# Performance work log

Hardware: AMD Instinct MI355X
Metric: run time of the kernel (lower is better)

## Reference

```python
import jax, jax.numpy as jnp
import numpy as np

N_NODES = 100000
N_EDGES = 1600000
IN_C, HID_C, OUT_C, N_CLS = 128, 128, 128, 40


def setup_inputs() -> dict:
    key = jax.random.key(0)
    ks = jax.random.split(key, 10)
    x = jax.random.normal(ks[0], (N_NODES, IN_C), dtype=jnp.float32)
    edge_index = jax.random.randint(ks[1], (2, N_EDGES), 0, N_NODES, dtype=jnp.int64)
    s = 1.0 / np.sqrt(IN_C)
    W_self1 = jax.random.uniform(ks[2], (IN_C, HID_C), jnp.float32, -s, s)
    W_neigh1 = jax.random.uniform(ks[3], (IN_C, HID_C), jnp.float32, -s, s)
    b1 = jnp.zeros((HID_C,), jnp.float32)
    s2 = 1.0 / np.sqrt(HID_C)
    W_self2 = jax.random.uniform(ks[4], (HID_C, OUT_C), jnp.float32, -s2, s2)
    W_neigh2 = jax.random.uniform(ks[5], (HID_C, OUT_C), jnp.float32, -s2, s2)
    b2 = jnp.zeros((OUT_C,), jnp.float32)
    s3 = 1.0 / np.sqrt(OUT_C)
    W_cls = jax.random.uniform(ks[6], (OUT_C, N_CLS), jnp.float32, -s3, s3)
    b_cls = jax.random.uniform(ks[7], (N_CLS,), jnp.float32, -s3, s3)
    return dict(x=x, edge_index=edge_index, W_self1=W_self1, W_neigh1=W_neigh1, b1=b1,
                W_self2=W_self2, W_neigh2=W_neigh2, b2=b2, W_cls=W_cls, b_cls=b_cls)


def _mean_agg(h, src, dst, n_nodes):
    # sum of in-neighbor features per destination node, then divide by in-degree
    sums = jax.ops.segment_sum(h[src], dst, num_segments=n_nodes)  # [N, F]
    deg = jax.ops.segment_sum(jnp.ones(src.shape[0], h.dtype), dst, num_segments=n_nodes)
    return sums / jnp.maximum(deg, 1.0)[:, None]


def _sage_conv(h, src, dst, W_self, W_neigh, b):
    # DGL mean SAGEConv: fc_self(h) + fc_neigh(mean_neigh(h)) + bias
    h_neigh = _mean_agg(h, src, dst, h.shape[0])
    return h @ W_self + h_neigh @ W_neigh + b


def reference(x, edge_index, W_self1, W_neigh1, b1, W_self2, W_neigh2, b2, W_cls, b_cls):
    src, dst = edge_index[0], edge_index[1]
    h = jax.nn.relu(_sage_conv(x, src, dst, W_self1, W_neigh1, b1))
    h = jax.nn.relu(_sage_conv(h, src, dst, W_self2, W_neigh2, b2))
    return h @ W_cls + b_cls
```

## Files before the change

### kernel.cpp

```cpp
#include <hip/hip_runtime.h>

#define N_NODES 100000
#define N_EDGES 1600000
#define C 128
#define NCLS 40
#define NBUCK 196
#define BCAP 12288
#define NT_TILES 3125

typedef _Float16 half8 __attribute__((ext_vector_type(8)));
typedef float f32x4 __attribute__((ext_vector_type(4)));
typedef float f32x16 __attribute__((ext_vector_type(16)));


__global__ __launch_bounds__(256) void bucket_scatter_k(const int* __restrict__ src,
    const int* __restrict__ dst, int* __restrict__ bucket_cnt, int* __restrict__ bucketArr) {
  __shared__ int lh[NBUCK], lbase[NBUCK], lcur[NBUCK];
  int tid = threadIdx.x;
  for (int i = tid; i < NBUCK; i += 256) { lh[i] = 0; lcur[i] = 0; }
  __syncthreads();
  int base = blockIdx.x * 4096;
  int bmax = min(base + 4096, N_EDGES);
  for (int e = base + tid; e < bmax; e += 256)
    atomicAdd(&lh[dst[e] >> 9], 1);
  __syncthreads();
  for (int i = tid; i < NBUCK; i += 256)
    lbase[i] = lh[i] ? atomicAdd(&bucket_cnt[i], lh[i]) : 0;
  __syncthreads();
  for (int e = base + tid; e < bmax; e += 256) {
    int d = dst[e];
    int b = d >> 9, loc = d & 511;
    int p = lbase[b] + atomicAdd(&lcur[b], 1);
    if (p < BCAP) bucketArr[(size_t)b * BCAP + p] = (src[e] << 9) | loc;
  }
}

__global__ void bucket_scan_k(const int* __restrict__ bucket_cnt, int* __restrict__ bucket_base,
                              int* __restrict__ rp) {
  if (threadIdx.x == 0 && blockIdx.x == 0) {
    int run = 0;
    for (int b = 0; b < NBUCK; b++) {
      bucket_base[b] = run;
      run += min(bucket_cnt[b], BCAP);
    }
    bucket_base[NBUCK] = run;
    rp[N_NODES] = run;
  }
}

__global__ __launch_bounds__(256) void bucket_sort_k(const int* __restrict__ bucketArr,
    const int* __restrict__ bucket_cnt, const int* __restrict__ bucket_base,
    int* __restrict__ rp, int* __restrict__ csr) {
  __shared__ int hist[512], offs[512], curs[512];
  __shared__ int wpart[4];
  __shared__ int lsrc[BCAP];
  int b = blockIdx.x, tid = threadIdx.x;
  int cnt = min(bucket_cnt[b], BCAP);
  int base = bucket_base[b];
  for (int i = tid; i < 512; i += 256) hist[i] = 0;
  __syncthreads();
  for (int i = tid; i < cnt; i += 256)
    atomicAdd(&hist[bucketArr[(size_t)b * BCAP + i] & 511], 1);
  __syncthreads();
  int a0 = hist[2 * tid], a1 = hist[2 * tid + 1];
  int s = a0 + a1;
  int lane = tid & 63, wid = tid >> 6;
  int inc = s;
  for (int d = 1; d < 64; d <<= 1) { int y = __shfl_up(inc, d, 64); if (lane >= d) inc += y; }
  if (lane == 63) wpart[wid] = inc;
  __syncthreads();
  int woff = 0;
  for (int q = 0; q < wid; q++) woff += wpart[q];
  int ex = woff + inc - s;
  offs[2 * tid] = ex; offs[2 * tid + 1] = ex + a0;
  curs[2 * tid] = ex; curs[2 * tid + 1] = ex + a0;
  __syncthreads();
  for (int i = tid; i < 512; i += 256) {
    int gn = b * 512 + i;
    if (gn < N_NODES) rp[gn] = base + offs[i];
  }
  for (int i = tid; i < cnt; i += 256) {
    int packed = bucketArr[(size_t)b * BCAP + i];
    int p = atomicAdd(&curs[packed & 511], 1);
    lsrc[p] = packed >> 9;
  }
  __syncthreads();
  for (int i = tid; i < cnt; i += 256) csr[base + i] = lsrc[i];
}


__global__ __launch_bounds__(256) void f32_to_f16_k(const float* __restrict__ in,
                                                    _Float16* __restrict__ out) {
  int i = blockIdx.x * 256 + threadIdx.x;
  float4 v0 = *(const float4*)(in + (size_t)i * 8);
  float4 v1 = *(const float4*)(in + (size_t)i * 8 + 4);
  half8 o;
  o[0] = (_Float16)v0.x; o[1] = (_Float16)v0.y; o[2] = (_Float16)v0.z; o[3] = (_Float16)v0.w;
  o[4] = (_Float16)v1.x; o[5] = (_Float16)v1.y; o[6] = (_Float16)v1.z; o[7] = (_Float16)v1.w;
  *(half8*)(out + (size_t)i * 8) = o;
}

__global__ void build_wt_k(const float* __restrict__ Ws, const float* __restrict__ Wn,
                           _Float16* __restrict__ WT) {
  int n = blockIdx.x, k = threadIdx.x;
  float v = (k < 128) ? Ws[k * 128 + n] : Wn[(k - 128) * 128 + n];
  WT[n * 256 + k] = (_Float16)v;
}

__global__ void build_wct_k(const float* __restrict__ Wc, const float* __restrict__ bc,
                            _Float16* __restrict__ WcT, float* __restrict__ bcf) {
  int c = blockIdx.x, k = threadIdx.x;
  float v = (c < NCLS) ? Wc[k * NCLS + c] : 0.f;
  WcT[c * C + k] = (_Float16)v;
  if (k == 0) bcf[c] = (c < NCLS) ? bc[c] : 0.f;
}


__global__ __launch_bounds__(256) void agg_mean_h_k(const _Float16* __restrict__ feat,
    const int* __restrict__ rp, const int* __restrict__ csr, _Float16* __restrict__ out) {
  int w = threadIdx.x >> 6;
  int node = blockIdx.x * 4 + w;
  int lane = threadIdx.x & 63;
  int g = lane >> 4, lr = lane & 15;
  int beg = rp[node], end = rp[node + 1];
  float acc[8] = {}, acc2[8] = {};
  int j = beg;
  for (; j + 8 <= end; j += 8) {
    int e0 = csr[j + g];
    int e1 = csr[j + 4 + g];
    half8 v0 = *(const half8*)(feat + (size_t)e0 * C + lr * 8);
    half8 v1 = *(const half8*)(feat + (size_t)e1 * C + lr * 8);
#pragma unroll
    for (int q = 0; q < 8; q++) { acc[q] += (float)v0[q]; acc2[q] += (float)v1[q]; }
  }
  for (; j + 4 <= end; j += 4) {
    int e0 = csr[j + g];
    half8 v0 = *(const half8*)(feat + (size_t)e0 * C + lr * 8);
#pragma unroll
    for (int q = 0; q < 8; q++) acc[q] += (float)v0[q];
  }
  int rem = end - j;
  if (g < rem) {
    int e0 = csr[j + g];
    half8 v0 = *(const half8*)(feat + (size_t)e0 * C + lr * 8);
#pragma unroll
    for (int q = 0; q < 8; q++) acc2[q] += (float)v0[q];
  }
#pragma unroll
  for (int q = 0; q < 8; q++) {
    float v = acc[q] + acc2[q];
    v += __shfl_xor(v, 16, 64);
    v += __shfl_xor(v, 32, 64);
    acc[q] = v;
  }
  if (g == 0) {
    float inv = 1.0f / fmaxf((float)(end - beg), 1.0f);
    half8 o;
#pragma unroll
    for (int q = 0; q < 8; q++) o[q] = (_Float16)(acc[q] * inv);
    *(half8*)(out + (size_t)node * C + lr * 8) = o;
  }
}


__global__ __launch_bounds__(256) void sage_gemm_ws_k(
    const _Float16* __restrict__ Xs, const _Float16* __restrict__ Xn,
    const _Float16* __restrict__ WT, const float* __restrict__ bias,
    _Float16* __restrict__ out) {
  __shared__ _Float16 cbuf[32][136];
  int tid = threadIdx.x, lane = tid & 63, wid = tid >> 6;
  int l31 = lane & 31, l5 = lane >> 5;
  int col0 = wid * 32;

  half8 b[16];
#pragma unroll
  for (int ks = 0; ks < 16; ks++)
    b[ks] = *(const half8*)(WT + (size_t)(col0 + l31) * 256 + ks * 16 + l5 * 8);
  float bcol = bias[col0 + l31];

  for (int t = blockIdx.x; t < NT_TILES; t += gridDim.x) {
    size_t row0 = (size_t)t * 32;
    half8 a[16];
#pragma unroll
    for (int ks = 0; ks < 8; ks++) {
      a[ks]     = *(const half8*)(Xs + (row0 + l31) * C + ks * 16 + l5 * 8);
      a[ks + 8] = *(const half8*)(Xn + (row0 + l31) * C + ks * 16 + l5 * 8);
    }
    f32x16 acc = {};
#pragma unroll
    for (int ks = 0; ks < 16; ks++)
      acc = __builtin_amdgcn_mfma_f32_32x32x16_f16(a[ks], b[ks], acc, 0, 0, 0);

    __syncthreads();
#pragma unroll
    for (int q = 0; q < 16; q++) {
      int row = (q & 3) + 8 * (q >> 2) + 4 * l5;
      float v = fmaxf(acc[q] + bcol, 0.f);
      cbuf[row][col0 + l31] = (_Float16)v;
    }
    __syncthreads();
#pragma unroll
    for (int p = 0; p < 2; p++) {
      int chunk = tid + p * 256;
      int r = chunk >> 4, cg = chunk & 15;
      half8 v = *(const half8*)&cbuf[r][cg * 8];
      *(half8*)(out + (row0 + r) * C + cg * 8) = v;
    }
  }
}


__global__ __launch_bounds__(256) void classifier_mfma_k(const _Float16* __restrict__ h,
    const _Float16* __restrict__ WcT, const float* __restrict__ bcf, float* __restrict__ out) {
  __shared__ float cbuf[64][49];
  int tid = threadIdx.x, lane = tid & 63, wid = tid >> 6;
  int lr = lane & 15, lk = lane >> 4;
  int row0 = blockIdx.x * 64 + wid * 16;
  f32x4 acc[3] = {};
#pragma unroll
  for (int ks = 0; ks < 4; ks++) {
    half8 a = {};
    int r = row0 + lr;
    if (r < N_NODES) a = *(const half8*)(h + (size_t)r * C + ks * 32 + lk * 8);
#pragma unroll
    for (int nf = 0; nf < 3; nf++) {
      half8 bfr = *(const half8*)(WcT + (size_t)(nf * 16 + lr) * C + ks * 32 + lk * 8);
      acc[nf] = __builtin_amdgcn_mfma_f32_16x16x32_f16(a, bfr, acc[nf], 0, 0, 0);
    }
  }
#pragma unroll
  for (int nf = 0; nf < 3; nf++)
#pragma unroll
    for (int q = 0; q < 4; q++) {
      int c = nf * 16 + lr;
      cbuf[wid * 16 + lk * 4 + q][c] = acc[nf][q] + bcf[c];
    }
  __syncthreads();
  int row_blk0 = blockIdx.x * 64;
  for (int i = tid; i < 64 * NCLS; i += 256) {
    int r = i / NCLS, c = i - r * NCLS;
    int gr = row_blk0 + r;
    if (gr < N_NODES) out[(size_t)gr * NCLS + c] = cbuf[r][c];
  }
}


extern "C" void kernel_launch(void* const* d_in, const int* in_sizes, int n_in,
                              void* d_out, int out_size, void* d_ws, size_t ws_size,
                              hipStream_t stream) {
  (void)in_sizes; (void)n_in; (void)out_size; (void)ws_size;
  const float* x   = (const float*)d_in[0];
  const int*   ei  = (const int*)d_in[1];
  const float* Ws1 = (const float*)d_in[2];
  const float* Wn1 = (const float*)d_in[3];
  const float* b1  = (const float*)d_in[4];
  const float* Ws2 = (const float*)d_in[5];
  const float* Wn2 = (const float*)d_in[6];
  const float* b2  = (const float*)d_in[7];
  const float* Wc  = (const float*)d_in[8];
  const float* bc  = (const float*)d_in[9];
  const int* src = ei;
  const int* dst = ei + N_EDGES;

  char* ws = (char*)d_ws;
  size_t off = 0;
  auto alloc = [&](size_t bytes) {
    void* p = ws + off;
    off = (off + bytes + 255) & ~(size_t)255;
    return p;
  };
  int*      bucket_cnt  = (int*)alloc((size_t)NBUCK * 4);
  int*      bucket_base = (int*)alloc((size_t)(NBUCK + 1) * 4);
  int*      bucketArr   = (int*)alloc((size_t)NBUCK * BCAP * 4);
  int*      rp          = (int*)alloc((size_t)(N_NODES + 1) * 4);
  int*      csr         = (int*)alloc((size_t)N_EDGES * 4);
  _Float16* hA          = (_Float16*)alloc((size_t)N_NODES * C * 2);
  _Float16* hB          = (_Float16*)alloc((size_t)N_NODES * C * 2);
  _Float16* hC          = (_Float16*)alloc((size_t)N_NODES * C * 2);
  _Float16* WT1         = (_Float16*)alloc((size_t)C * 256 * 2);
  _Float16* WT2         = (_Float16*)alloc((size_t)C * 256 * 2);
  _Float16* WcT         = (_Float16*)alloc((size_t)48 * C * 2);
  float*    bcf         = (float*)alloc(48 * 4);
  float* outf = (float*)d_out;

  hipMemsetAsync(bucket_cnt, 0, (size_t)NBUCK * 4, stream);
  bucket_scatter_k<<<(N_EDGES + 4095) / 4096, 256, 0, stream>>>(src, dst, bucket_cnt, bucketArr);
  bucket_scan_k<<<1, 64, 0, stream>>>(bucket_cnt, bucket_base, rp);
  bucket_sort_k<<<NBUCK, 256, 0, stream>>>(bucketArr, bucket_cnt, bucket_base, rp, csr);

  build_wt_k<<<C, 256, 0, stream>>>(Ws1, Wn1, WT1);
  build_wt_k<<<C, 256, 0, stream>>>(Ws2, Wn2, WT2);
  build_wct_k<<<48, C, 0, stream>>>(Wc, bc, WcT, bcf);
  f32_to_f16_k<<<(N_NODES * C / 8) / 256, 256, 0, stream>>>(x, hA);

  agg_mean_h_k<<<N_NODES / 4, 256, 0, stream>>>(hA, rp, csr, hB);
  sage_gemm_ws_k<<<782, 256, 0, stream>>>(hA, hB, WT1, b1, hC);
  agg_mean_h_k<<<N_NODES / 4, 256, 0, stream>>>(hC, rp, csr, hB);
  sage_gemm_ws_k<<<782, 256, 0, stream>>>(hC, hB, WT2, b2, hA);
  classifier_mfma_k<<<(N_NODES + 63) / 64, 256, 0, stream>>>(hA, WcT, bcf, outf);
}
```

Measured before the change: 371.8 us.

## Shard mean aggregation by feature column across XCD-mapped blocks; parallelize bucket scan

Result: slower. 436.7 us (+17.4%).

```diff
diff --git a/kernel.cpp b/kernel.cpp
--- a/kernel.cpp
+++ b/kernel.cpp
@@ -21,14 +21,17 @@
   __syncthreads();
   int base = blockIdx.x * 4096;
   int bmax = min(base + 4096, N_EDGES);
-  for (int e = base + tid; e < bmax; e += 256)
-    atomicAdd(&lh[dst[e] >> 9], 1);
+  int dreg[16];
+  int nk = 0;
+  for (int e = base + tid; e < bmax; e += 256) dreg[nk++] = dst[e];
+  for (int k = 0; k < nk; k++) atomicAdd(&lh[dreg[k] >> 9], 1);
   __syncthreads();
   for (int i = tid; i < NBUCK; i += 256)
     lbase[i] = lh[i] ? atomicAdd(&bucket_cnt[i], lh[i]) : 0;
   __syncthreads();
+  nk = 0;
   for (int e = base + tid; e < bmax; e += 256) {
-    int d = dst[e];
+    int d = dreg[nk++];
     int b = d >> 9, loc = d & 511;
     int p = lbase[b] + atomicAdd(&lcur[b], 1);
     if (p < BCAP) bucketArr[(size_t)b * BCAP + p] = (src[e] << 9) | loc;
@@ -37,15 +40,19 @@
 
 __global__ void bucket_scan_k(const int* __restrict__ bucket_cnt, int* __restrict__ bucket_base,
                               int* __restrict__ rp) {
-  if (threadIdx.x == 0 && blockIdx.x == 0) {
-    int run = 0;
-    for (int b = 0; b < NBUCK; b++) {
-      bucket_base[b] = run;
-      run += min(bucket_cnt[b], BCAP);
-    }
-    bucket_base[NBUCK] = run;
-    rp[N_NODES] = run;
-  }
+  int tid = threadIdx.x;
+  int v = (tid < NBUCK) ? min(bucket_cnt[tid], BCAP) : 0;
+  int lane = tid & 63, wid = tid >> 6;
+  int inc = v;
+  for (int d = 1; d < 64; d <<= 1) { int y = __shfl_up(inc, d, 64); if (lane >= d) inc += y; }
+  __shared__ int wsum[4];
+  if (lane == 63) wsum[wid] = inc;
+  __syncthreads();
+  int woff = 0;
+  for (int q = 0; q < wid; q++) woff += wsum[q];
+  int ex = woff + inc - v;
+  if (tid < NBUCK) bucket_base[tid] = ex;
+  if (tid == NBUCK - 1) { bucket_base[NBUCK] = ex + v; rp[N_NODES] = ex + v; }
 }
 
 __global__ __launch_bounds__(256) void bucket_sort_k(const int* __restrict__ bucketArr,
@@ -116,41 +123,48 @@
 }
 
 
-__global__ __launch_bounds__(256) void agg_mean_h_k(const _Float16* __restrict__ feat,
+__global__ __launch_bounds__(256) void agg_mean_shard_k(const _Float16* __restrict__ feat,
     const int* __restrict__ rp, const int* __restrict__ csr, _Float16* __restrict__ out) {
-  int w = threadIdx.x >> 6;
-  int node = blockIdx.x * 4 + w;
-  int lane = threadIdx.x & 63;
-  int g = lane >> 4, lr = lane & 15;
+  int bid = blockIdx.x;
+  int shard = (bid & 7) >> 1;
+  int tile  = (bid >> 3) * 2 + (bid & 1);
+  int tid = threadIdx.x;
+  int w = tid >> 6, lane = tid & 63;
+  int nslot = lane >> 4;
+  int g  = (lane >> 2) & 3;
+  int lr = lane & 3;
+  int node = tile * 16 + w * 4 + nslot;
   int beg = rp[node], end = rp[node + 1];
+  const _Float16* fbase = feat + shard * 32 + lr * 8;
   float acc[8] = {}, acc2[8] = {};
   int j = beg;
   for (; j + 8 <= end; j += 8) {
     int e0 = csr[j + g];
     int e1 = csr[j + 4 + g];
-    half8 v0 = *(const half8*)(feat + (size_t)e0 * C + lr * 8);
-    half8 v1 = *(const half8*)(feat + (size_t)e1 * C + lr * 8);
+    half8 v0 = *(const half8*)(fbase + (size_t)e0 * C);
+    half8 v1 = *(const half8*)(fbase + (size_t)e1 * C);
 #pragma unroll
     for (int q = 0; q < 8; q++) { acc[q] += (float)v0[q]; acc2[q] += (float)v1[q]; }
   }
-  for (; j + 4 <= end; j += 4) {
+  if (j + 4 <= end) {
     int e0 = csr[j + g];
-    half8 v0 = *(const half8*)(feat + (size_t)e0 * C + lr * 8);
+    half8 v0 = *(const half8*)(fbase + (size_t)e0 * C);
 #pragma unroll
     for (int q = 0; q < 8; q++) acc[q] += (float)v0[q];
+    j += 4;
   }
   int rem = end - j;
   if (g < rem) {
     int e0 = csr[j + g];
-    half8 v0 = *(const half8*)(feat + (size_t)e0 * C + lr * 8);
+    half8 v0 = *(const half8*)(fbase + (size_t)e0 * C);
 #pragma unroll
     for (int q = 0; q < 8; q++) acc2[q] += (float)v0[q];
   }
 #pragma unroll
   for (int q = 0; q < 8; q++) {
     float v = acc[q] + acc2[q];
-    v += __shfl_xor(v, 16, 64);
-    v += __shfl_xor(v, 32, 64);
+    v += __shfl_xor(v, 4, 64);
+    v += __shfl_xor(v, 8, 64);
     acc[q] = v;
   }
   if (g == 0) {
@@ -158,7 +172,7 @@
     half8 o;
 #pragma unroll
     for (int q = 0; q < 8; q++) o[q] = (_Float16)(acc[q] * inv);
-    *(half8*)(out + (size_t)node * C + lr * 8) = o;
+    *(half8*)(out + (size_t)node * C + shard * 32 + lr * 8) = o;
   }
 }
 
@@ -285,7 +299,7 @@
 
   hipMemsetAsync(bucket_cnt, 0, (size_t)NBUCK * 4, stream);
   bucket_scatter_k<<<(N_EDGES + 4095) / 4096, 256, 0, stream>>>(src, dst, bucket_cnt, bucketArr);
-  bucket_scan_k<<<1, 64, 0, stream>>>(bucket_cnt, bucket_base, rp);
+  bucket_scan_k<<<1, 256, 0, stream>>>(bucket_cnt, bucket_base, rp);
   bucket_sort_k<<<NBUCK, 256, 0, stream>>>(bucketArr, bucket_cnt, bucket_base, rp, csr);
 
   build_wt_k<<<C, 256, 0, stream>>>(Ws1, Wn1, WT1);
@@ -293,9 +307,9 @@
   build_wct_k<<<48, C, 0, stream>>>(Wc, bc, WcT, bcf);
   f32_to_f16_k<<<(N_NODES * C / 8) / 256, 256, 0, stream>>>(x, hA);
 
-  agg_mean_h_k<<<N_NODES / 4, 256, 0, stream>>>(hA, rp, csr, hB);
+  agg_mean_shard_k<<<25000, 256, 0, stream>>>(hA, rp, csr, hB);
   sage_gemm_ws_k<<<782, 256, 0, stream>>>(hA, hB, WT1, b1, hC);
-  agg_mean_h_k<<<N_NODES / 4, 256, 0, stream>>>(hC, rp, csr, hB);
+  agg_mean_shard_k<<<25000, 256, 0, stream>>>(hC, rp, csr, hB);
   sage_gemm_ws_k<<<782, 256, 0, stream>>>(hC, hB, WT2, b2, hA);
   classifier_mfma_k<<<(N_NODES + 63) / 64, 256, 0, stream>>>(hA, WcT, bcf, outf);
 }
```
